# Kernel tuning notes

Measured on AMD Instinct MI355X. Metric: run time of the kernel, lower is better.

Reference implementation:

```python
import jax, jax.numpy as jnp
import numpy as np

D = 1024  # dim_context


def setup_inputs() -> dict:
    key = jax.random.key(0)
    k1, k2, k3, k4, k5 = jax.random.split(key, 5)
    B, T = 32, 2048
    hidden = jax.random.normal(k1, (B, D), dtype=jnp.float32)
    encoder_outputs = jax.random.normal(k2, (B, T, D), dtype=jnp.float32)
    # nn.Linear(2D, D): weight [D, 2D], bias [D]
    lim = 1.0 / np.sqrt(2 * D)
    W = jax.random.uniform(k3, (D, 2 * D), minval=-lim, maxval=lim, dtype=jnp.float32)
    b = jax.random.uniform(k4, (D,), minval=-lim, maxval=lim, dtype=jnp.float32)
    stdv = 1.0 / np.sqrt(D)
    v = jax.random.uniform(k5, (D,), minval=-stdv, maxval=stdv, dtype=jnp.float32)
    return {"hidden": hidden, "encoder_outputs": encoder_outputs, "W": W, "b": b, "v": v}


def reference(hidden, encoder_outputs, W, b, v):
    # hidden: [B, D]; encoder_outputs: [B, T, D]
    B, T, Dm = encoder_outputs.shape
    h = jnp.broadcast_to(hidden[:, None, :], (B, T, Dm))      # repeat over T
    attn_inputs = jnp.concatenate([h, encoder_outputs], axis=2)  # [B, T, 2D]
    energy = jax.nn.relu(jnp.einsum('btk,dk->btd', attn_inputs, W) + b)  # [B, T, D]
    scores = jnp.einsum('btd,d->bt', energy, v)                # [B, T]
    # softmax over dim=1 (time axis), then unsqueeze(1)
    return jax.nn.softmax(scores, axis=1)[:, None, :]          # [B, 1, T]
```

## Files before the change

### kernel.cpp

```cpp
#include <hip/hip_runtime.h>
#include <cstdint>


#define GLOBAL_AS __attribute__((address_space(1)))
#define LDS_AS    __attribute__((address_space(3)))

typedef __bf16 bf16x8 __attribute__((ext_vector_type(8)));
typedef float  f32x4  __attribute__((ext_vector_type(4)));

__device__ __forceinline__ unsigned int f2bf(float x) {
    unsigned int u = __builtin_bit_cast(unsigned int, x);
    u += 0x7fffu + ((u >> 16) & 1u);
    return u >> 16;
}

__global__ __launch_bounds__(256) void k_convert_enc(const float4* __restrict__ in,
                                                     uint4* __restrict__ out) {
    size_t idx = (size_t)blockIdx.x * 256 + threadIdx.x;
    float4 f0 = in[idx * 2];
    float4 f1 = in[idx * 2 + 1];
    uint4 o;
    o.x = f2bf(f0.x) | (f2bf(f0.y) << 16);
    o.y = f2bf(f0.z) | (f2bf(f0.w) << 16);
    o.z = f2bf(f1.x) | (f2bf(f1.y) << 16);
    o.w = f2bf(f1.z) | (f2bf(f1.w) << 16);
    out[idx] = o;
}

__global__ __launch_bounds__(256) void k_convert_we(const float* __restrict__ W,
                                                    uint2* __restrict__ out) {
    int idx = blockIdx.x * 256 + threadIdx.x;
    int i = idx * 4;
    int n = i >> 10, k = i & 1023;
    const float4 f = *(const float4*)(W + (size_t)n * 2048 + 1024 + k);
    uint2 o;
    o.x = f2bf(f.x) | (f2bf(f.y) << 16);
    o.y = f2bf(f.z) | (f2bf(f.w) << 16);
    out[idx] = o;
}

__global__ __launch_bounds__(256) void k_hidden_proj(const float* __restrict__ hidden,
                                                     const float* __restrict__ W,
                                                     const float* __restrict__ bias,
                                                     float* __restrict__ u) {
    __shared__ float wrow[1024];
    __shared__ float red[256];
    const int tid = threadIdx.x, d = blockIdx.x;
    ((float4*)wrow)[tid] = ((const float4*)(W + (size_t)d * 2048))[tid];
    __syncthreads();
    const int b = tid & 31, kc = tid >> 5;
    const float* h = hidden + b * 1024 + kc * 128;
    const float* w = wrow + kc * 128;
    float acc = 0.f;
    #pragma unroll 8
    for (int i = 0; i < 128; i += 4) {
        float4 hv = *(const float4*)(h + i);
        acc += w[i] * hv.x + w[i + 1] * hv.y + w[i + 2] * hv.z + w[i + 3] * hv.w;
    }
    red[tid] = acc;
    __syncthreads();
    if (tid < 32) {
        float s = 0.f;
        #pragma unroll
        for (int j = 0; j < 8; j++) s += red[j * 32 + tid];
        u[tid * 1024 + d] = s + bias[d];
    }
}

__global__ __launch_bounds__(256, 4) void k_gemm_score(
        const unsigned short* __restrict__ Ab,
        const unsigned short* __restrict__ Bw,
        const float* __restrict__ u,
        const float* __restrict__ v,
        float* __restrict__ scores2) {
    constexpr int K = 1024, BK = 64;
    __shared__ __align__(16) unsigned short As[128 * BK];
    __shared__ __align__(16) unsigned short Bs[128 * BK];
    __shared__ float red[2][128];

    const int tid  = threadIdx.x;
    const int wave = tid >> 6;
    const int lane = tid & 63;
    const int mb   = blockIdx.x;
    const int z    = blockIdx.y;
    const int wm = wave & 1, wn = wave >> 1;
    const int q = lane >> 4, cl = lane & 15;

    int aoff[4], boff[4];
    #pragma unroll
    for (int i = 0; i < 4; i++) {
        int ra = wm * 64 + i * 16 + cl;
        aoff[i] = ra * 64 + ((q ^ (ra & 7)) << 3);
        int rb = wn * 64 + i * 16 + cl;
        boff[i] = rb * 64 + ((q ^ (rb & 7)) << 3);
    }

    int soff[4];
    #pragma unroll
    for (int c = 0; c < 4; c++) {
        int row = (wave * 4 + c) * 8 + (lane >> 3);
        int g   = (lane & 7) ^ (row & 7);
        soff[c] = row * K + g * 8;
    }
    const unsigned short* Abase = Ab + (size_t)(mb * 128) * K;

    float sacc[4][4];
    #pragma unroll
    for (int i = 0; i < 4; i++)
        #pragma unroll
        for (int r = 0; r < 4; r++) sacc[i][r] = 0.f;

    const int bidx = mb >> 4;
    f32x4 acc[4][4];

    for (int p = 0; p < 4; p++) {
        const int nb = z * 4 + p;
        const unsigned short* Bbase = Bw + (size_t)(nb * 128) * K;
        #pragma unroll
        for (int i = 0; i < 4; i++)
            #pragma unroll
            for (int j = 0; j < 4; j++) acc[i][j] = (f32x4){0.f, 0.f, 0.f, 0.f};

        for (int k0 = 0; k0 < K; k0 += BK) {
            #pragma unroll
            for (int c = 0; c < 4; c++) {
                const int chunk = wave * 4 + c;
                __builtin_amdgcn_global_load_lds(
                    (GLOBAL_AS void*)(size_t)(Abase + soff[c] + k0),
                    (LDS_AS void*)(As + chunk * 512), 16, 0, 0);
                __builtin_amdgcn_global_load_lds(
                    (GLOBAL_AS void*)(size_t)(Bbase + soff[c] + k0),
                    (LDS_AS void*)(Bs + chunk * 512), 16, 0, 0);
            }
            __syncthreads();
            #pragma unroll
            for (int h = 0; h < 2; h++) {
                const int hx = h * 32;
                bf16x8 afr[4], bfr[4];
                #pragma unroll
                for (int i = 0; i < 4; i++) afr[i] = *(const bf16x8*)(As + (aoff[i] ^ hx));
                #pragma unroll
                for (int j = 0; j < 4; j++) bfr[j] = *(const bf16x8*)(Bs + (boff[j] ^ hx));
                #pragma unroll
                for (int i = 0; i < 4; i++)
                    #pragma unroll
                    for (int j = 0; j < 4; j++)
                        acc[i][j] = __builtin_amdgcn_mfma_f32_16x16x32_bf16(afr[i], bfr[j], acc[i][j], 0, 0, 0);
            }
            __syncthreads();
        }

        float vv[4], uu[4];
        #pragma unroll
        for (int j = 0; j < 4; j++) {
            int n = nb * 128 + wn * 64 + j * 16 + cl;
            vv[j] = v[n];
            uu[j] = u[bidx * 1024 + n];
        }
        #pragma unroll
        for (int i = 0; i < 4; i++)
            #pragma unroll
            for (int r = 0; r < 4; r++) {
                float s = sacc[i][r];
                #pragma unroll
                for (int j = 0; j < 4; j++)
                    s += fmaxf(acc[i][j][r] + uu[j], 0.f) * vv[j];
                sacc[i][r] = s;
            }
    }

    #pragma unroll
    for (int i = 0; i < 4; i++)
        #pragma unroll
        for (int r = 0; r < 4; r++) {
            float s = sacc[i][r];
            s += __shfl_xor(s, 1);
            s += __shfl_xor(s, 2);
            s += __shfl_xor(s, 4);
            s += __shfl_xor(s, 8);
            if (cl == 0) red[wn][wm * 64 + i * 16 + q * 4 + r] = s;
        }
    __syncthreads();
    if (tid < 128) scores2[(size_t)z * 65536 + mb * 128 + tid] = red[0][tid] + red[1][tid];
}

__global__ __launch_bounds__(256) void k_softmax(const float* __restrict__ scores2,
                                                 float* __restrict__ out) {
    __shared__ float red[4];
    int b = blockIdx.x;
    int t0 = threadIdx.x;
    int wave = threadIdx.x >> 6, lane = threadIdx.x & 63;
    const float* s0 = scores2 + b * 2048;
    const float* s1 = scores2 + 65536 + b * 2048;
    float vals[8];
    float lmax = -1e30f;
    #pragma unroll
    for (int i = 0; i < 8; i++) {
        int t = t0 + i * 256;
        vals[i] = s0[t] + s1[t];
        lmax = fmaxf(lmax, vals[i]);
    }
    for (int o = 32; o > 0; o >>= 1) lmax = fmaxf(lmax, __shfl_xor(lmax, o));
    if (lane == 0) red[wave] = lmax;
    __syncthreads();
    float gmax = fmaxf(fmaxf(red[0], red[1]), fmaxf(red[2], red[3]));
    float lsum = 0.f;
    #pragma unroll
    for (int i = 0; i < 8; i++) {
        vals[i] = expf(vals[i] - gmax);
        lsum += vals[i];
    }
    for (int o = 32; o > 0; o >>= 1) lsum += __shfl_xor(lsum, o);
    __syncthreads();
    if (lane == 0) red[wave] = lsum;
    __syncthreads();
    float inv = 1.0f / (red[0] + red[1] + red[2] + red[3]);
    #pragma unroll
    for (int i = 0; i < 8; i++) out[b * 2048 + t0 + i * 256] = vals[i] * inv;
}

extern "C" void kernel_launch(void* const* d_in, const int* in_sizes, int n_in,
                              void* d_out, int out_size, void* d_ws, size_t ws_size,
                              hipStream_t stream) {
    const float* hidden = (const float*)d_in[0];
    const float* enc    = (const float*)d_in[1];
    const float* W      = (const float*)d_in[2];
    const float* bias   = (const float*)d_in[3];
    const float* v      = (const float*)d_in[4];
    float* out = (float*)d_out;

    char* ws = (char*)d_ws;
    unsigned short* encb = (unsigned short*)ws;
    unsigned short* Web  = (unsigned short*)(ws + 134217728);
    float* u       = (float*)(ws + 134217728 + 2097152);
    float* scores2 = (float*)(ws + 134217728 + 2097152 + 131072);

    k_convert_enc<<<32768, 256, 0, stream>>>((const float4*)enc, (uint4*)encb);
    k_convert_we<<<1024, 256, 0, stream>>>(W, (uint2*)Web);
    k_hidden_proj<<<1024, 256, 0, stream>>>(hidden, W, bias, u);
    dim3 g(512, 2);
    k_gemm_score<<<g, 256, 0, stream>>>(encb, Web, u, v, scores2);
    k_softmax<<<32, 256, 0, stream>>>(scores2, out);
}
```

Before: 559.5 us.

## Fuse prep kernels into one launch and split GEMM N across four blocks

Merges the encoder conversion, W conversion and hidden projection into a single block-dispatched prep kernel, which saves two launches. The encoder conversion now uses a coalesced uint2 store pattern. The score GEMM grid grows from 2 to 4 N-splits, each block covering 2 N-tiles instead of 4, to raise parallelism. Softmax then sums four partial score buffers. The extra split rereads the A tile from memory twice as often.

```diff
diff --git a/kernel.cpp b/kernel.cpp
--- a/kernel.cpp
+++ b/kernel.cpp
@@ -14,56 +14,58 @@
     return u >> 16;
 }
 
-__global__ __launch_bounds__(256) void k_convert_enc(const float4* __restrict__ in,
-                                                     uint4* __restrict__ out) {
-    size_t idx = (size_t)blockIdx.x * 256 + threadIdx.x;
-    float4 f0 = in[idx * 2];
-    float4 f1 = in[idx * 2 + 1];
-    uint4 o;
-    o.x = f2bf(f0.x) | (f2bf(f0.y) << 16);
-    o.y = f2bf(f0.z) | (f2bf(f0.w) << 16);
-    o.z = f2bf(f1.x) | (f2bf(f1.y) << 16);
-    o.w = f2bf(f1.z) | (f2bf(f1.w) << 16);
-    out[idx] = o;
-}
-
-__global__ __launch_bounds__(256) void k_convert_we(const float* __restrict__ W,
-                                                    uint2* __restrict__ out) {
-    int idx = blockIdx.x * 256 + threadIdx.x;
-    int i = idx * 4;
-    int n = i >> 10, k = i & 1023;
-    const float4 f = *(const float4*)(W + (size_t)n * 2048 + 1024 + k);
-    uint2 o;
-    o.x = f2bf(f.x) | (f2bf(f.y) << 16);
-    o.y = f2bf(f.z) | (f2bf(f.w) << 16);
-    out[idx] = o;
-}
-
-__global__ __launch_bounds__(256) void k_hidden_proj(const float* __restrict__ hidden,
-                                                     const float* __restrict__ W,
-                                                     const float* __restrict__ bias,
-                                                     float* __restrict__ u) {
-    __shared__ float wrow[1024];
-    __shared__ float red[256];
-    const int tid = threadIdx.x, d = blockIdx.x;
-    ((float4*)wrow)[tid] = ((const float4*)(W + (size_t)d * 2048))[tid];
-    __syncthreads();
-    const int b = tid & 31, kc = tid >> 5;
-    const float* h = hidden + b * 1024 + kc * 128;
-    const float* w = wrow + kc * 128;
-    float acc = 0.f;
-    #pragma unroll 8
-    for (int i = 0; i < 128; i += 4) {
-        float4 hv = *(const float4*)(h + i);
-        acc += w[i] * hv.x + w[i + 1] * hv.y + w[i + 2] * hv.z + w[i + 3] * hv.w;
-    }
-    red[tid] = acc;
-    __syncthreads();
-    if (tid < 32) {
-        float s = 0.f;
-        #pragma unroll
-        for (int j = 0; j < 8; j++) s += red[j * 32 + tid];
-        u[tid * 1024 + d] = s + bias[d];
+__global__ __launch_bounds__(256) void k_prep(const float4* __restrict__ enc4,
+                                              uint2* __restrict__ encb2,
+                                              const float* __restrict__ W,
+                                              uint2* __restrict__ Web2,
+                                              const float* __restrict__ hidden,
+                                              const float* __restrict__ bias,
+                                              float* __restrict__ u) {
+    __shared__ float sh[1024 + 256];
+    const int bid = blockIdx.x, tid = threadIdx.x;
+    if (bid < 32768) {
+        const size_t base4 = (size_t)bid * 512 + (tid >> 6) * 128 + (tid & 63);
+        float4 f0 = enc4[base4];
+        float4 f1 = enc4[base4 + 64];
+        uint2 o0, o1;
+        o0.x = f2bf(f0.x) | (f2bf(f0.y) << 16);
+        o0.y = f2bf(f0.z) | (f2bf(f0.w) << 16);
+        o1.x = f2bf(f1.x) | (f2bf(f1.y) << 16);
+        o1.y = f2bf(f1.z) | (f2bf(f1.w) << 16);
+        encb2[base4] = o0;
+        encb2[base4 + 64] = o1;
+    } else if (bid < 33792) {
+        int idx = (bid - 32768) * 256 + tid;
+        int i = idx * 4;
+        int n = i >> 10, k = i & 1023;
+        const float4 f = *(const float4*)(W + (size_t)n * 2048 + 1024 + k);
+        uint2 o;
+        o.x = f2bf(f.x) | (f2bf(f.y) << 16);
+        o.y = f2bf(f.z) | (f2bf(f.w) << 16);
+        Web2[idx] = o;
+    } else {
+        const int d = bid - 33792;
+        float* wrow = sh;
+        float* red  = sh + 1024;
+        ((float4*)wrow)[tid] = ((const float4*)(W + (size_t)d * 2048))[tid];
+        __syncthreads();
+        const int b = tid & 31, kc = tid >> 5;
+        const float* h = hidden + b * 1024 + kc * 128;
+        const float* w = wrow + kc * 128;
+        float acc = 0.f;
+        #pragma unroll 8
+        for (int i = 0; i < 128; i += 4) {
+            float4 hv = *(const float4*)(h + i);
+            acc += w[i] * hv.x + w[i + 1] * hv.y + w[i + 2] * hv.z + w[i + 3] * hv.w;
+        }
+        red[tid] = acc;
+        __syncthreads();
+        if (tid < 32) {
+            float s = 0.f;
+            #pragma unroll
+            for (int j = 0; j < 8; j++) s += red[j * 32 + tid];
+            u[tid * 1024 + d] = s + bias[d];
+        }
     }
 }
 
@@ -72,7 +74,7 @@
         const unsigned short* __restrict__ Bw,
         const float* __restrict__ u,
         const float* __restrict__ v,
-        float* __restrict__ scores2) {
+        float* __restrict__ scores4) {
     constexpr int K = 1024, BK = 64;
     __shared__ __align__(16) unsigned short As[128 * BK];
     __shared__ __align__(16) unsigned short Bs[128 * BK];
@@ -113,8 +115,8 @@
     const int bidx = mb >> 4;
     f32x4 acc[4][4];
 
-    for (int p = 0; p < 4; p++) {
-        const int nb = z * 4 + p;
+    for (int p = 0; p < 2; p++) {
+        const int nb = z * 2 + p;
         const unsigned short* Bbase = Bw + (size_t)(nb * 128) * K;
         #pragma unroll
         for (int i = 0; i < 4; i++)
@@ -181,23 +183,25 @@
             if (cl == 0) red[wn][wm * 64 + i * 16 + q * 4 + r] = s;
         }
     __syncthreads();
-    if (tid < 128) scores2[(size_t)z * 65536 + mb * 128 + tid] = red[0][tid] + red[1][tid];
-}
-
-__global__ __launch_bounds__(256) void k_softmax(const float* __restrict__ scores2,
+    if (tid < 128) scores4[(size_t)z * 65536 + mb * 128 + tid] = red[0][tid] + red[1][tid];
+}
+
+__global__ __launch_bounds__(256) void k_softmax(const float* __restrict__ scores4,
                                                  float* __restrict__ out) {
     __shared__ float red[4];
     int b = blockIdx.x;
     int t0 = threadIdx.x;
     int wave = threadIdx.x >> 6, lane = threadIdx.x & 63;
-    const float* s0 = scores2 + b * 2048;
-    const float* s1 = scores2 + 65536 + b * 2048;
+    const float* s0 = scores4 + b * 2048;
+    const float* s1 = scores4 + 65536 + b * 2048;
+    const float* s2 = scores4 + 131072 + b * 2048;
+    const float* s3 = scores4 + 196608 + b * 2048;
     float vals[8];
     float lmax = -1e30f;
     #pragma unroll
     for (int i = 0; i < 8; i++) {
         int t = t0 + i * 256;
-        vals[i] = s0[t] + s1[t];
+        vals[i] = (s0[t] + s1[t]) + (s2[t] + s3[t]);
         lmax = fmaxf(lmax, vals[i]);
     }
     for (int o = 32; o > 0; o >>= 1) lmax = fmaxf(lmax, __shfl_xor(lmax, o));
@@ -233,12 +237,11 @@
     unsigned short* encb = (unsigned short*)ws;
     unsigned short* Web  = (unsigned short*)(ws + 134217728);
     float* u       = (float*)(ws + 134217728 + 2097152);
-    float* scores2 = (float*)(ws + 134217728 + 2097152 + 131072);
-
-    k_convert_enc<<<32768, 256, 0, stream>>>((const float4*)enc, (uint4*)encb);
-    k_convert_we<<<1024, 256, 0, stream>>>(W, (uint2*)Web);
-    k_hidden_proj<<<1024, 256, 0, stream>>>(hidden, W, bias, u);
-    dim3 g(512, 2);
-    k_gemm_score<<<g, 256, 0, stream>>>(encb, Web, u, v, scores2);
-    k_softmax<<<32, 256, 0, stream>>>(scores2, out);
-}
+    float* scores4 = (float*)(ws + 134217728 + 2097152 + 131072);
+
+    k_prep<<<34816, 256, 0, stream>>>((const float4*)enc, (uint2*)encb,
+                                      W, (uint2*)Web, hidden, bias, u);
+    dim3 g(512, 4);
+    k_gemm_score<<<g, 256, 0, stream>>>(encb, Web, u, v, scores4);
+    k_softmax<<<32, 256, 0, stream>>>(scores4, out);
+}
```

After: 662.3 us. +18.4%, slower.
